# Kernel optimization log

Hardware: AMD Instinct MI355X
Metric: run time of the kernel (lower is better)

## Reference

```python
import jax, jax.numpy as jnp
import numpy as np

N = 10000      # nodes
E = 160000     # edges
D_IN = 512
D_H = 512
P_DROP = 0.2


def _glorot(key, shape):
    lim = float(np.sqrt(6.0 / (shape[0] + shape[1])))
    return jax.random.uniform(key, shape, jnp.float32, -lim, lim)


def setup_inputs() -> dict:
    key = jax.random.key(0)
    ks = jax.random.split(key, 8)
    h = jax.random.normal(ks[0], (N, D_IN), jnp.float32)
    src = jax.random.randint(ks[1], (E,), 0, N)
    dst = jax.random.randint(ks[2], (E,), 0, N)
    edge_weight = jax.random.uniform(ks[3], (E,), jnp.float32)
    W0 = _glorot(ks[4], (D_IN, D_H))
    W1 = _glorot(ks[5], (D_H, D_H))
    W2 = _glorot(ks[6], (D_H, D_H))
    b0 = jnp.zeros((D_H,), jnp.float32)
    b1 = jnp.zeros((D_H,), jnp.float32)
    b2 = jnp.zeros((D_H,), jnp.float32)
    return dict(h=h, src=src, dst=dst, edge_weight=edge_weight,
                W0=W0, b0=b0, W1=W1, b1=b1, W2=W2, b2=b2)


def _dropout(x, key):
    keep = jax.random.bernoulli(key, 1.0 - P_DROP, x.shape)
    return jnp.where(keep, x / (1.0 - P_DROP), 0.0)


def _graph_conv(x, src, dst, ew, W, b, act):
    # DGL GraphConv, norm='both', weight=True, bias=True, with edge_weight.
    ones = jnp.ones((src.shape[0],), x.dtype)
    deg_out = jnp.maximum(jax.ops.segment_sum(ones, src, num_segments=N), 1.0)
    deg_in = jnp.maximum(jax.ops.segment_sum(ones, dst, num_segments=N), 1.0)
    x = x * (deg_out ** -0.5)[:, None]          # src norm
    msg = x[src] * ew[:, None]                  # [E, D] gather + edge weight
    agg = jax.ops.segment_sum(msg, dst, num_segments=N)  # scatter-add
    out = (agg @ W) * (deg_in ** -0.5)[:, None] + b
    return act(out) if act is not None else out


def reference(h, src, dst, edge_weight, W0, b0, W1, b1, W2, b2):
    dk = jax.random.split(jax.random.key(42), 3)
    x = _dropout(h, dk[0])
    x = _graph_conv(x, src, dst, edge_weight, W0, b0, jax.nn.elu)
    x = _dropout(x, dk[1])
    x = _graph_conv(x, src, dst, edge_weight, W1, b1, jax.nn.elu)
    x = _dropout(x, dk[2])
    x = _graph_conv(x, src, dst, edge_weight, W2, b2, None)
    return x
```

## Files before the change

kernel.cpp:

```cpp
#include <hip/hip_runtime.h>
#include <stdint.h>

#define N_NODES 10000
#define N_EDGES 160000
#define D 512
#define TOT (N_NODES * D)
#define M_PAD 10112

typedef _Float16 h8 __attribute__((ext_vector_type(8)));
typedef float f4 __attribute__((ext_vector_type(4)));

__host__ __device__ inline uint32_t rotl32(uint32_t v, int r) {
    return (v << r) | (v >> (32 - r));
}

__host__ __device__ inline void tf2x32(uint32_t k0, uint32_t k1,
                                       uint32_t& x0, uint32_t& x1) {
    uint32_t k2 = k0 ^ k1 ^ 0x1BD11BDAu;
    x0 += k0; x1 += k1;
    x0 += x1; x1 = rotl32(x1, 13); x1 ^= x0;
    x0 += x1; x1 = rotl32(x1, 15); x1 ^= x0;
    x0 += x1; x1 = rotl32(x1, 26); x1 ^= x0;
    x0 += x1; x1 = rotl32(x1,  6); x1 ^= x0;
    x0 += k1; x1 += k2 + 1u;
    x0 += x1; x1 = rotl32(x1, 17); x1 ^= x0;
    x0 += x1; x1 = rotl32(x1, 29); x1 ^= x0;
    x0 += x1; x1 = rotl32(x1, 16); x1 ^= x0;
    x0 += x1; x1 = rotl32(x1, 24); x1 ^= x0;
    x0 += k2; x1 += k0 + 2u;
    x0 += x1; x1 = rotl32(x1, 13); x1 ^= x0;
    x0 += x1; x1 = rotl32(x1, 15); x1 ^= x0;
    x0 += x1; x1 = rotl32(x1, 26); x1 ^= x0;
    x0 += x1; x1 = rotl32(x1,  6); x1 ^= x0;
    x0 += k0; x1 += k1 + 3u;
    x0 += x1; x1 = rotl32(x1, 17); x1 ^= x0;
    x0 += x1; x1 = rotl32(x1, 29); x1 ^= x0;
    x0 += x1; x1 = rotl32(x1, 16); x1 ^= x0;
    x0 += x1; x1 = rotl32(x1, 24); x1 ^= x0;
    x0 += k1; x1 += k2 + 4u;
    x0 += x1; x1 = rotl32(x1, 13); x1 ^= x0;
    x0 += x1; x1 = rotl32(x1, 15); x1 ^= x0;
    x0 += x1; x1 = rotl32(x1, 26); x1 ^= x0;
    x0 += x1; x1 = rotl32(x1,  6); x1 ^= x0;
    x0 += k2; x1 += k0 + 5u;
}

__device__ __forceinline__ float dropout_gate(uint32_t k0, uint32_t k1, uint32_t j) {
    uint32_t c0 = 0u, c1 = j;
    tf2x32(k0, k1, c0, c1);
    uint32_t bits = c0 ^ c1;
    float u = __uint_as_float((bits >> 9) | 0x3f800000u) - 1.0f;
    return (u < 0.8f) ? 1.0f : 0.0f;
}

__global__ void hist_kernel(const int* __restrict__ src, const int* __restrict__ dst,
                            int* __restrict__ deg_out, int* __restrict__ deg_in) {
    int e = blockIdx.x * 256 + threadIdx.x;
    if (e >= N_EDGES) return;
    atomicAdd(&deg_out[src[e]], 1);
    atomicAdd(&deg_in[dst[e]], 1);
}

__global__ __launch_bounds__(1024)
void scan_kernel(const int* __restrict__ deg_in, const int* __restrict__ deg_out,
                 int* __restrict__ row_ptr,
                 float* __restrict__ rn_in, float* __restrict__ rn_out) {
    __shared__ int wsum[16];
    __shared__ int base_s;
    int tid = threadIdx.x;
    int lane = tid & 63, wv = tid >> 6;
    if (tid == 0) base_s = 0;
    __syncthreads();
    for (int start = 0; start < N_NODES; start += 1024) {
        int i = start + tid;
        int v = (i < N_NODES) ? deg_in[i] : 0;
        int s = v;
#pragma unroll
        for (int off = 1; off < 64; off <<= 1) {
            int t = __shfl_up(s, off, 64);
            if (lane >= off) s += t;
        }
        if (lane == 63) wsum[wv] = s;
        __syncthreads();
        if (wv == 0 && lane < 16) {
            int ws = wsum[lane];
#pragma unroll
            for (int off = 1; off < 16; off <<= 1) {
                int t = __shfl_up(ws, off, 64);
                if (lane >= off) ws += t;
            }
            wsum[lane] = ws;
        }
        __syncthreads();
        if (i < N_NODES) {
            int prefix = base_s + ((wv > 0) ? wsum[wv - 1] : 0) + (s - v);
            row_ptr[i] = prefix;
            rn_in[i]  = 1.0f / sqrtf(fmaxf((float)v, 1.0f));
            rn_out[i] = 1.0f / sqrtf(fmaxf((float)deg_out[i], 1.0f));
        }
        __syncthreads();
        if (tid == 0) base_s += wsum[15];
        __syncthreads();
    }
    if (tid == 0) row_ptr[N_NODES] = base_s;
}

__global__ void fill_kernel(const int* __restrict__ src, const int* __restrict__ dst,
                            const float* __restrict__ ew, const int* __restrict__ row_ptr,
                            int* __restrict__ cursor, int2* __restrict__ csr) {
    int e = blockIdx.x * 256 + threadIdx.x;
    if (e >= N_EDGES) return;
    int v = dst[e];
    int pos = atomicAdd(&cursor[v], 1);
    int idx = row_ptr[v] + pos;
    csr[idx] = make_int2(src[e], __float_as_int(ew[e]));
}

__global__ __launch_bounds__(256)
void wconvert_kernel(const float* __restrict__ W0, const float* __restrict__ W1,
                     const float* __restrict__ W2, _Float16* __restrict__ Wt) {
    __shared__ float tile[64][65];
    const float* W = (blockIdx.z == 0) ? W0 : (blockIdx.z == 1) ? W1 : W2;
    _Float16* T = Wt + (size_t)blockIdx.z * 512 * 512;
    int r0 = blockIdx.y * 64, c0 = blockIdx.x * 64;
    int t = threadIdx.x;
    int c = t & 63, rq = t >> 6;
#pragma unroll
    for (int i = 0; i < 16; ++i) {
        int r = rq + i * 4;
        tile[r][c] = W[(size_t)(r0 + r) * 512 + c0 + c];
    }
    __syncthreads();
    int k = t & 63, nq = t >> 6;
#pragma unroll
    for (int i = 0; i < 16; ++i) {
        int n = nq + i * 4;
        T[(size_t)(c0 + n) * 512 + r0 + k] = (_Float16)tile[k][n];
    }
}

__global__ __launch_bounds__(256)
void dropout_kernel(const float* __restrict__ x, _Float16* __restrict__ y,
                    const float* __restrict__ rn_out, uint32_t k0, uint32_t k1) {
    int t = blockIdx.x * 256 + threadIdx.x;
    int j = t * 4;
    if (j >= TOT) return;
    float4 xv = *(const float4*)&x[j];
    float w = rn_out[j >> 9];
    _Float16 r[4];
    uint32_t jj = (uint32_t)j;
#pragma unroll
    for (int i = 0; i < 4; ++i) {
        float g = dropout_gate(k0, k1, jj + (uint32_t)i);
        float xi = (&xv.x)[i];
        r[i] = (_Float16)(g * (xi / 0.8f) * w);
    }
    *(ushort4*)&y[j] = *(ushort4*)r;
}

__global__ __launch_bounds__(256)
void dropout16_kernel(const _Float16* __restrict__ x, _Float16* __restrict__ y,
                      const float* __restrict__ rn_out, uint32_t k0, uint32_t k1) {
    int t = blockIdx.x * 256 + threadIdx.x;
    int j = t * 8;
    if (j >= TOT) return;
    h8 xv = *(const h8*)&x[j];
    float w = rn_out[j >> 9];
    _Float16 r[8];
    uint32_t jj = (uint32_t)j;
#pragma unroll
    for (int i = 0; i < 8; ++i) {
        float g = dropout_gate(k0, k1, jj + (uint32_t)i);
        r[i] = (_Float16)(g * ((float)xv[i] / 0.8f) * w);
    }
    *(h8*)&y[j] = *(h8*)r;
}

__global__ __launch_bounds__(256)
void aggregate_kernel(const _Float16* __restrict__ y, const int* __restrict__ row_ptr,
                      const int2* __restrict__ csr, _Float16* __restrict__ agg) {
    int node = blockIdx.x * 4 + (threadIdx.x >> 6);
    int lane = threadIdx.x & 63;
    if (node >= N_NODES) return;
    int beg = row_ptr[node], end = row_ptr[node + 1];
    float acc[8] = {0, 0, 0, 0, 0, 0, 0, 0};
    int k = beg;
    for (; k + 7 < end; k += 8) {
        h8 a[8];
        float w[8];
#pragma unroll
        for (int q = 0; q < 8; ++q) {
            int2 e = csr[k + q];
            a[q] = *(const h8*)&y[(size_t)e.x * 512 + lane * 8];
            w[q] = __int_as_float(e.y);
        }
#pragma unroll
        for (int q = 0; q < 8; ++q)
#pragma unroll
            for (int i = 0; i < 8; ++i) acc[i] += w[q] * (float)a[q][i];
    }
    for (; k + 3 < end; k += 4) {
        h8 a[4];
        float w[4];
#pragma unroll
        for (int q = 0; q < 4; ++q) {
            int2 e = csr[k + q];
            a[q] = *(const h8*)&y[(size_t)e.x * 512 + lane * 8];
            w[q] = __int_as_float(e.y);
        }
#pragma unroll
        for (int q = 0; q < 4; ++q)
#pragma unroll
            for (int i = 0; i < 8; ++i) acc[i] += w[q] * (float)a[q][i];
    }
    for (; k < end; ++k) {
        int2 e0 = csr[k];
        float w0 = __int_as_float(e0.y);
        h8 a = *(const h8*)&y[(size_t)e0.x * 512 + lane * 8];
#pragma unroll
        for (int i = 0; i < 8; ++i) acc[i] += w0 * (float)a[i];
    }
    _Float16 r[8];
#pragma unroll
    for (int i = 0; i < 8; ++i) r[i] = (_Float16)acc[i];
    *(h8*)&agg[(size_t)node * 512 + lane * 8] = *(h8*)r;
}

#define GBK 32
#define LDA 40
__global__ __launch_bounds__(256)
void gemm_kernel(const _Float16* __restrict__ A, const _Float16* __restrict__ Wt,
                 const float* __restrict__ bias, const float* __restrict__ rn_in,
                 _Float16* __restrict__ yout, float* __restrict__ fout, int mode) {
    __shared__ _Float16 As[128 * LDA];
    int tid = threadIdx.x;
    int wv = tid >> 6, lane = tid & 63;

    int f = blockIdx.x + blockIdx.y * 8;
    int T = (f & 7) * 79 + (f >> 3);
    int row0 = (T >> 3) * 128, col0 = (T & 7) * 64;

    int wr = wv >> 1, wc = wv & 1;

    f4 acc[4][2];
#pragma unroll
    for (int i = 0; i < 4; ++i)
#pragma unroll
        for (int j = 0; j < 2; ++j) acc[i][j] = (f4){0.f, 0.f, 0.f, 0.f};

    int srow = tid >> 2;
    int sseg = (tid & 3) * 8;
    const _Float16* gA0 = A + (size_t)(row0 + srow) * 512 + sseg;
    const _Float16* gA1 = gA0 + (size_t)64 * 512;
    _Float16* wA0 = &As[srow * LDA + sseg];
    _Float16* wA1 = &As[(64 + srow) * LDA + sseg];

    int kf = (lane >> 4) * 8;
    const _Float16* fa = &As[(wr * 64 + (lane & 15)) * LDA + kf];
    const _Float16* gB0 = Wt + (size_t)(col0 + wc * 32 + (lane & 15)) * 512 + kf;
    const _Float16* gB1 = gB0 + (size_t)16 * 512;

    h8 ra0 = *(const h8*)gA0;
    h8 ra1 = *(const h8*)gA1;
    h8 rb0 = *(const h8*)gB0;
    h8 rb1 = *(const h8*)gB1;

    for (int kk = 0; kk < 512; kk += GBK) {
        *(h8*)wA0 = ra0;
        *(h8*)wA1 = ra1;
        h8 bf0 = rb0, bf1 = rb1;
        __syncthreads();
        if (kk + GBK < 512) {
            ra0 = *(const h8*)(gA0 + kk + GBK);
            ra1 = *(const h8*)(gA1 + kk + GBK);
            rb0 = *(const h8*)(gB0 + kk + GBK);
            rb1 = *(const h8*)(gB1 + kk + GBK);
        }
        h8 af[4];
#pragma unroll
        for (int mt = 0; mt < 4; ++mt) af[mt] = *(const h8*)(fa + mt * 16 * LDA);
#pragma unroll
        for (int mt = 0; mt < 4; ++mt) {
            acc[mt][0] = __builtin_amdgcn_mfma_f32_16x16x32_f16(af[mt], bf0,
                                                                acc[mt][0], 0, 0, 0);
            acc[mt][1] = __builtin_amdgcn_mfma_f32_16x16x32_f16(af[mt], bf1,
                                                                acc[mt][1], 0, 0, 0);
        }
        __syncthreads();
    }

    int mbase = row0 + wr * 64;
    int nbase = col0 + wc * 32;
#pragma unroll
    for (int mt = 0; mt < 4; ++mt) {
#pragma unroll
        for (int nt = 0; nt < 2; ++nt) {
            int gr0 = mbase + mt * 16 + (lane >> 4) * 4;
            int gc = nbase + nt * 16 + (lane & 15);
            float bcol = bias[gc];
#pragma unroll
            for (int i = 0; i < 4; ++i) {
                int gr = gr0 + i;
                if (gr >= N_NODES) continue;
                float v = acc[mt][nt][i] * rn_in[gr] + bcol;
                if (mode == 0) {
                    v = (v > 0.f) ? v : expm1f(v);
                    yout[(size_t)gr * 512 + gc] = (_Float16)v;
                } else {
                    fout[(size_t)gr * 512 + gc] = v;
                }
            }
        }
    }
}

extern "C" void kernel_launch(void* const* d_in, const int* in_sizes, int n_in,
                              void* d_out, int out_size, void* d_ws, size_t ws_size,
                              hipStream_t stream) {
    const float* h   = (const float*)d_in[0];
    const int*   src = (const int*)d_in[1];
    const int*   dst = (const int*)d_in[2];
    const float* ew  = (const float*)d_in[3];
    const float* W0  = (const float*)d_in[4];
    const float* b0  = (const float*)d_in[5];
    const float* W1  = (const float*)d_in[6];
    const float* b1  = (const float*)d_in[7];
    const float* W2  = (const float*)d_in[8];
    const float* b2  = (const float*)d_in[9];
    const float* bl[3] = {b0, b1, b2};
    float* out = (float*)d_out;

    char* ws = (char*)d_ws;
    _Float16* y16  = (_Float16*)ws; ws += (size_t)TOT * 2;
    _Float16* yPre = (_Float16*)ws; ws += (size_t)TOT * 2;
    _Float16* aggF = (_Float16*)ws; ws += (size_t)M_PAD * 512 * 2;
    _Float16* Wt   = (_Float16*)ws; ws += (size_t)3 * 512 * 512 * 2;
    int* degi_in  = (int*)ws;  ws += N_NODES * 4;
    int* degi_out = (int*)ws;  ws += N_NODES * 4;
    int* cursor   = (int*)ws;  ws += N_NODES * 4;
    int* row_ptr  = (int*)ws;  ws += (N_NODES + 1) * 4;
    ws = (char*)(((uintptr_t)ws + 15) & ~(uintptr_t)15);
    int2* csr     = (int2*)ws; ws += (size_t)N_EDGES * 8;
    float* rn_in  = (float*)ws; ws += N_NODES * 4;
    float* rn_out = (float*)ws; ws += N_NODES * 4;

    hipMemsetAsync(degi_in, 0, 3 * N_NODES * 4, stream);

    hist_kernel<<<(N_EDGES + 255) / 256, 256, 0, stream>>>(src, dst, degi_out, degi_in);
    scan_kernel<<<1, 1024, 0, stream>>>(degi_in, degi_out, row_ptr, rn_in, rn_out);
    fill_kernel<<<(N_EDGES + 255) / 256, 256, 0, stream>>>(src, dst, ew, row_ptr,
                                                           cursor, csr);
    wconvert_kernel<<<dim3(8, 8, 3), 256, 0, stream>>>(W0, W1, W2, Wt);

    uint32_t dk[3][2];
    for (int i = 0; i < 3; ++i) {
        uint32_t c0 = 0u, c1 = (uint32_t)i;
        tf2x32(0u, 42u, c0, c1);
        dk[i][0] = c0; dk[i][1] = c1;
    }

    dropout_kernel<<<(TOT / 4 + 255) / 256, 256, 0, stream>>>(h, y16, rn_out,
                                                              dk[0][0], dk[0][1]);
    for (int l = 0; l < 3; ++l) {
        aggregate_kernel<<<N_NODES / 4, 256, 0, stream>>>(y16, row_ptr, csr, aggF);
        int mode = (l < 2) ? 0 : 1;
        gemm_kernel<<<dim3(8, M_PAD / 128), 256, 0, stream>>>(
            aggF, Wt + (size_t)l * 512 * 512, bl[l], rn_in, yPre, out, mode);
        if (l < 2) {
            dropout16_kernel<<<TOT / 8 / 256, 256, 0, stream>>>(
                yPre, y16, rn_out, dk[l + 1][0], dk[l + 1][1]);
        }
    }
}
```

Baseline: 319.6 us.

## Precompute packed dropout bitmasks and fuse dropout into GEMM epilogue

A new mask kernel builds the Threefry dropout masks for the two hidden layers up front, packed one bit per element. The GEMM epilogue for layers 0 and 1 then applies the mask, the 1/0.8 scale and the out-degree normalisation, and writes straight into the next layer's input buffer. This drops the separate dropout16 passes and the yPre intermediate, avoiding a full fp16 read and write per layer. In exchange the epilogue does extra scattered mask and rn_out loads, and the RNG work moves into one earlier kernel.

```diff
diff --git a/kernel.cpp b/kernel.cpp
--- a/kernel.cpp
+++ b/kernel.cpp
@@ -6,6 +6,7 @@
 #define D 512
 #define TOT (N_NODES * D)
 #define M_PAD 10112
+#define MASK_DW (TOT / 32)
 
 typedef _Float16 h8 __attribute__((ext_vector_type(8)));
 typedef float f4 __attribute__((ext_vector_type(4)));
@@ -53,6 +54,26 @@
     return (u < 0.8f) ? 1.0f : 0.0f;
 }
 
+__global__ __launch_bounds__(256)
+void mask_kernel(uint32_t* __restrict__ mask, uint32_t k0a, uint32_t k1a,
+                 uint32_t k0b, uint32_t k1b) {
+    int t = blockIdx.x * 256 + threadIdx.x;
+    int layer = (t >= MASK_DW) ? 1 : 0;
+    uint32_t k0 = layer ? k0b : k0a;
+    uint32_t k1 = layer ? k1b : k1a;
+    uint32_t base = (uint32_t)(layer ? t - MASK_DW : t) * 32u;
+    uint32_t m = 0;
+#pragma unroll
+    for (int i = 0; i < 32; ++i) {
+        uint32_t c0 = 0u, c1 = base + (uint32_t)i;
+        tf2x32(k0, k1, c0, c1);
+        uint32_t bits = c0 ^ c1;
+        float u = __uint_as_float((bits >> 9) | 0x3f800000u) - 1.0f;
+        m |= (u < 0.8f ? 1u : 0u) << i;
+    }
+    mask[t] = m;
+}
+
 __global__ void hist_kernel(const int* __restrict__ src, const int* __restrict__ dst,
                             int* __restrict__ deg_out, int* __restrict__ deg_in) {
     int e = blockIdx.x * 256 + threadIdx.x;
@@ -159,24 +180,6 @@
 }
 
 __global__ __launch_bounds__(256)
-void dropout16_kernel(const _Float16* __restrict__ x, _Float16* __restrict__ y,
-                      const float* __restrict__ rn_out, uint32_t k0, uint32_t k1) {
-    int t = blockIdx.x * 256 + threadIdx.x;
-    int j = t * 8;
-    if (j >= TOT) return;
-    h8 xv = *(const h8*)&x[j];
-    float w = rn_out[j >> 9];
-    _Float16 r[8];
-    uint32_t jj = (uint32_t)j;
-#pragma unroll
-    for (int i = 0; i < 8; ++i) {
-        float g = dropout_gate(k0, k1, jj + (uint32_t)i);
-        r[i] = (_Float16)(g * ((float)xv[i] / 0.8f) * w);
-    }
-    *(h8*)&y[j] = *(h8*)r;
-}
-
-__global__ __launch_bounds__(256)
 void aggregate_kernel(const _Float16* __restrict__ y, const int* __restrict__ row_ptr,
                       const int2* __restrict__ csr, _Float16* __restrict__ agg) {
     int node = blockIdx.x * 4 + (threadIdx.x >> 6);
@@ -231,6 +234,7 @@
 __global__ __launch_bounds__(256)
 void gemm_kernel(const _Float16* __restrict__ A, const _Float16* __restrict__ Wt,
                  const float* __restrict__ bias, const float* __restrict__ rn_in,
+                 const float* __restrict__ rn_out, const uint32_t* __restrict__ mask,
                  _Float16* __restrict__ yout, float* __restrict__ fout, int mode) {
     __shared__ _Float16 As[128 * LDA];
     int tid = threadIdx.x;
@@ -305,6 +309,9 @@
                 float v = acc[mt][nt][i] * rn_in[gr] + bcol;
                 if (mode == 0) {
                     v = (v > 0.f) ? v : expm1f(v);
+                    uint32_t m = mask[gr * 16 + (gc >> 5)];
+                    float keep = (float)((m >> (gc & 31)) & 1u);
+                    v = keep * (v / 0.8f) * rn_out[gr];
                     yout[(size_t)gr * 512 + gc] = (_Float16)v;
                 } else {
                     fout[(size_t)gr * 512 + gc] = v;
@@ -332,9 +339,9 @@
 
     char* ws = (char*)d_ws;
     _Float16* y16  = (_Float16*)ws; ws += (size_t)TOT * 2;
-    _Float16* yPre = (_Float16*)ws; ws += (size_t)TOT * 2;
     _Float16* aggF = (_Float16*)ws; ws += (size_t)M_PAD * 512 * 2;
     _Float16* Wt   = (_Float16*)ws; ws += (size_t)3 * 512 * 512 * 2;
+    uint32_t* mask = (uint32_t*)ws; ws += (size_t)2 * MASK_DW * 4;
     int* degi_in  = (int*)ws;  ws += N_NODES * 4;
     int* degi_out = (int*)ws;  ws += N_NODES * 4;
     int* cursor   = (int*)ws;  ws += N_NODES * 4;
@@ -346,18 +353,20 @@
 
     hipMemsetAsync(degi_in, 0, 3 * N_NODES * 4, stream);
 
+    uint32_t dk[3][2];
+    for (int i = 0; i < 3; ++i) {
+        uint32_t c0 = 0u, c1 = (uint32_t)i;
+        tf2x32(0u, 42u, c0, c1);
+        dk[i][0] = c0; dk[i][1] = c1;
+    }
+
+    mask_kernel<<<(2 * MASK_DW) / 256, 256, 0, stream>>>(mask, dk[1][0], dk[1][1],
+                                                         dk[2][0], dk[2][1]);
     hist_kernel<<<(N_EDGES + 255) / 256, 256, 0, stream>>>(src, dst, degi_out, degi_in);
     scan_kernel<<<1, 1024, 0, stream>>>(degi_in, degi_out, row_ptr, rn_in, rn_out);
     fill_kernel<<<(N_EDGES + 255) / 256, 256, 0, stream>>>(src, dst, ew, row_ptr,
                                                            cursor, csr);
     wconvert_kernel<<<dim3(8, 8, 3), 256, 0, stream>>>(W0, W1, W2, Wt);
-
-    uint32_t dk[3][2];
-    for (int i = 0; i < 3; ++i) {
-        uint32_t c0 = 0u, c1 = (uint32_t)i;
-        tf2x32(0u, 42u, c0, c1);
-        dk[i][0] = c0; dk[i][1] = c1;
-    }
 
     dropout_kernel<<<(TOT / 4 + 255) / 256, 256, 0, stream>>>(h, y16, rn_out,
                                                               dk[0][0], dk[0][1]);
@@ -365,10 +374,7 @@
         aggregate_kernel<<<N_NODES / 4, 256, 0, stream>>>(y16, row_ptr, csr, aggF);
         int mode = (l < 2) ? 0 : 1;
         gemm_kernel<<<dim3(8, M_PAD / 128), 256, 0, stream>>>(
-            aggF, Wt + (size_t)l * 512 * 512, bl[l], rn_in, yPre, out, mode);
-        if (l < 2) {
-            dropout16_kernel<<<TOT / 8 / 256, 256, 0, stream>>>(
-                yPre, y16, rn_out, dk[l + 1][0], dk[l + 1][1]);
-        }
-    }
-}
+            aggF, Wt + (size_t)l * 512 * 512, bl[l], rn_in, rn_out,
+            mask + (size_t)l * MASK_DW, y16, out, mode);
+    }
+}
```

New measurement: 324.6 us. About the same (+1.6%).
